# Kernel optimization log

Hardware: AMD Instinct MI355X
Metric: run time of the kernel (lower is better)

Reference implementation:

```python
import jax, jax.numpy as jnp
import numpy as np
from jax import lax

BN_EPS = 1e-5


def binary_activation(x):
    # STE: forward = sign(x), backward = piecewise polynomial approximation
    out_fwd = jnp.sign(x)
    m1 = (x < -1).astype(x.dtype)
    m2 = (x < 0).astype(x.dtype)
    m3 = (x < 1).astype(x.dtype)
    out1 = -1.0 * m1 + (x * x + 2 * x) * (1 - m1)
    out2 = out1 * m2 + (-x * x + 2 * x) * (1 - m2)
    out3 = out2 * m3 + 1.0 * (1 - m3)
    return lax.stop_gradient(out_fwd) - lax.stop_gradient(out3) + out3


def binarize_weight(w):
    # per-output-channel scale * sign(w), STE through clipped weights
    scale = lax.stop_gradient(jnp.mean(jnp.abs(w), axis=(1, 2, 3), keepdims=True))
    bw_ng = scale * jnp.sign(w)
    wc = jnp.clip(w, -1.0, 1.0)
    return lax.stop_gradient(bw_ng) - lax.stop_gradient(wc) + wc


def conv3x3(x, w):
    return lax.conv_general_dilated(
        x, w, window_strides=(1, 1), padding=((1, 1), (1, 1)),
        dimension_numbers=('NCHW', 'OIHW', 'NCHW'))


def shift4(x, amt):
    # chunk into 4 along channel; roll +-amt over H for first two, over W for last two
    x1, x2, x3, x4 = jnp.split(x, 4, axis=1)
    return jnp.concatenate([
        jnp.roll(x1, amt, axis=2),
        jnp.roll(x2, -amt, axis=2),
        jnp.roll(x3, amt, axis=3),
        jnp.roll(x4, -amt, axis=3),
    ], axis=1)


def setup_inputs() -> dict:
    key = jax.random.key(0)
    ks = jax.random.split(key, 8)
    B, C, H, W = 32, 256, 56, 56
    x = jax.random.normal(ks[0], (B, C, H, W), dtype=jnp.float32)
    w0 = jax.random.uniform(ks[1], (C, C, 3, 3), dtype=jnp.float32) * 0.001
    w1 = jax.random.uniform(ks[2], (C, C, 3, 3), dtype=jnp.float32) * 0.001
    w2 = jax.random.uniform(ks[3], (C, C, 3, 3), dtype=jnp.float32) * 0.001
    return {
        'x': x,
        'bias0': jnp.zeros((1, C, 1, 1), jnp.float32),
        'w0': w0, 'w1': w1, 'w2': w2,
        'gamma': jnp.ones((C,), jnp.float32),
        'beta': jnp.zeros((C,), jnp.float32),
        'rmean': jnp.zeros((C,), jnp.float32),
        'rvar': jnp.ones((C,), jnp.float32),
        'bias1': jnp.zeros((1, C, 1, 1), jnp.float32),
        'prelu_a': 0.25 * jnp.ones((C,), jnp.float32),
        'bias2': jnp.zeros((1, C, 1, 1), jnp.float32),
    }


def reference(x, bias0, w0, w1, w2, gamma, beta, rmean, rvar, bias1, prelu_a, bias2):
    residual = x
    out = binary_activation(x + bias0)
    out1 = conv3x3(out, binarize_weight(w0))
    out2 = conv3x3(shift4(out, 1), binarize_weight(w1))   # Shift: roll by 1
    out3 = conv3x3(shift4(out, 3), binarize_weight(w2))   # GlobalShift: roll by 3
    s = out1 + out2 + out3
    # BatchNorm2d (inference mode with running stats)
    c = (1, -1, 1, 1)
    bn = (s - rmean.reshape(c)) * (gamma.reshape(c) * lax.rsqrt(rvar.reshape(c) + BN_EPS)) + beta.reshape(c)
    out = bn + residual
    out = out + bias1
    a = prelu_a.reshape(c)
    out = jnp.where(out > 0, out, a * out)  # PReLU, per-channel slope
    out = out + bias2
    return out
```

## Files before the change

kernel.cpp:

```cpp
#include <hip/hip_runtime.h>
#include <stdint.h>

#define BB 32
#define CC 256
#define HH 56
#define WW 56
#define TAPS 9
#define NCONV 3
#define BN_EPS 1e-5f

typedef int   int4v __attribute__((ext_vector_type(4)));
typedef float f16v  __attribute__((ext_vector_type(16)));

#define MFMA_FP4(accv, av, bv) \
    asm("v_mfma_f32_32x32x64_f8f6f4 %0, %1, %2, %0 cbsz:4 blgp:4" \
        : "+v"(accv) : "v"(av), "v"(bv))

#define ACT4_BYTES ((size_t)BB * HH * WW * 128)
#define WPK4_BYTES ((size_t)NCONV * 8 * 4 * TAPS * 64 * 16)
#define OT4_STRIDE 36864

#define L_PX   32
#define L_ROW  (58 * L_PX)
#define L_G    (4 * L_ROW)
#define NST4   464
#define SWZ(c) ((((c) ^ ((c) >> 2)) & 3) << 4)

__global__ __launch_bounds__(256) void pack_act4_kernel(
    const float* __restrict__ x, const float* __restrict__ bias0,
    uint8_t* __restrict__ act4)
{
    __shared__ uint8_t nib[56 * 260];
    const int tid = threadIdx.x;
    const int h = blockIdx.x % HH, n = blockIdx.x / HH;
    const int w = tid & 63;
    const int cq = tid >> 6;
    if (w < WW) {
        #pragma unroll 4
        for (int cc = 0; cc < 64; ++cc) {
            const int c = cc * 4 + cq;
            const float v = x[((size_t)(n * CC + c) * HH + h) * WW + w] + bias0[c];
            nib[w * 260 + c] = (v > 0.f) ? 0x2 : ((v < 0.f) ? 0xA : 0x0);
        }
    }
    __syncthreads();
    uint32_t* o32 = (uint32_t*)(act4 + (size_t)(n * HH + h) * WW * 128);
    #pragma unroll
    for (int i = 0; i < 7; ++i) {
        const int flat = i * 1024 + tid * 4;
        const int ww = flat >> 7, b0 = flat & 127;
        uint32_t r = 0;
        #pragma unroll
        for (int k = 0; k < 4; ++k) {
            const int b = b0 + k;
            const uint32_t lo = nib[ww * 260 + 2 * b];
            const uint32_t hi = nib[ww * 260 + 2 * b + 1];
            r |= ((lo | (hi << 4)) & 0xFFu) << (8 * k);
        }
        o32[flat >> 2] = r;
    }
}

__global__ __launch_bounds__(64) void pack_scales_kernel(
    const float* __restrict__ w0, const float* __restrict__ w1,
    const float* __restrict__ w2, float* __restrict__ scales,
    const float* __restrict__ gamma, const float* __restrict__ beta,
    const float* __restrict__ rmean, const float* __restrict__ rvar,
    const float* __restrict__ bias1, const float* __restrict__ prelu_a,
    const float* __restrict__ bias2, float* __restrict__ epack)
{
    const int j = blockIdx.x >> 8;
    const int o = blockIdx.x & 255;
    const float* wp = (j == 0) ? w0 : ((j == 1) ? w1 : w2);
    const int lane = threadIdx.x;
    const float* wo = wp + (size_t)o * CC * TAPS;
    float s = 0.f;
    for (int k = lane; k < CC * TAPS; k += 64) s += fabsf(wo[k]);
    #pragma unroll
    for (int d = 32; d > 0; d >>= 1) s += __shfl_xor(s, d);
    if (lane == 0) scales[j * CC + o] = s * (1.0f / (float)(CC * TAPS));
    if (j == 0 && lane == 0) {
        const float A = gamma[o] * rsqrtf(rvar[o] + BN_EPS);
        epack[o * 4 + 0] = A;
        epack[o * 4 + 1] = beta[o] - rmean[o] * A + bias1[o];
        epack[o * 4 + 2] = prelu_a[o];
        epack[o * 4 + 3] = bias2[o];
    }
}

__global__ __launch_bounds__(256) void pack_wpk4_kernel(
    const float* __restrict__ w0, const float* __restrict__ w1,
    const float* __restrict__ w2, uint8_t* __restrict__ wpk)
{
    const int j  = blockIdx.x >> 3;
    const int ot = blockIdx.x & 7;
    const float* wp = (j == 0) ? w0 : ((j == 1) ? w1 : w2);
    #pragma unroll 1
    for (int it = 0; it < 9; ++it) {
        const int e = it * 256 + threadIdx.x;
        const int g = e / 576;
        const int rem = e % 576;
        const int t = rem >> 6;
        const int ln = rem & 63;
        const int o = ot * 32 + (ln & 31);
        const int chb = g * 64 + ((ln >> 5) & 1) * 32;
        uint8_t bytes[16];
        #pragma unroll
        for (int b = 0; b < 16; ++b) {
            const float vlo = wp[((size_t)o * CC + chb + 2 * b) * TAPS + t];
            const float vhi = wp[((size_t)o * CC + chb + 2 * b + 1) * TAPS + t];
            const uint8_t nlo = (vlo > 0.f) ? 0x2 : ((vlo < 0.f) ? 0xA : 0x0);
            const uint8_t nhi = (vhi > 0.f) ? 0x2 : ((vhi < 0.f) ? 0xA : 0x0);
            bytes[b] = (uint8_t)(nlo | (nhi << 4));
        }
        *(int4v*)(wpk + ((size_t)((j * 8 + ot) * 4 + g) * 9 + t) * 1024 + ln * 16)
            = *(const int4v*)bytes;
    }
}

__global__ __launch_bounds__(256) void conv_mfma4_kernel(
    const uint8_t* __restrict__ act4, const uint8_t* __restrict__ wpk,
    const float* __restrict__ scales, const float* __restrict__ epack,
    const float* __restrict__ x, float* __restrict__ out)
{
    __shared__ __align__(16) uint8_t lds[2][L_G];
    const int tid  = threadIdx.x;
    const int lane = tid & 63;
    const int wv   = __builtin_amdgcn_readfirstlane(tid >> 6);
    const int bid  = blockIdx.x;
    const int swz  = (bid & 7) * 196 + (bid >> 3);
    const int pxblk = swz % 49;
    const int n     = swz / 49;
    const int px0   = pxblk * 64;
    const int h_lo  = px0 / WW;

    int boff[2][3];
    #pragma unroll
    for (int pt = 0; pt < 2; ++pt) {
        const int p = px0 + pt * 32 + (lane & 31);
        const int hl = p / WW, wl = p % WW;
        #pragma unroll
        for (int tc = 0; tc < 3; ++tc) {
            const int col = wl + tc;
            const int a = (hl - h_lo) * L_ROW + col * L_PX + ((lane >> 5) & 1) * 16;
            boff[pt][tc] = a ^ SWZ(col);
        }
    }
    const size_t nbase = (size_t)n * HH;

    float fsum[2][2][16];
    #pragma unroll
    for (int q = 0; q < 2; ++q)
        #pragma unroll
        for (int pt = 0; pt < 2; ++pt)
            #pragma unroll
            for (int r = 0; r < 16; ++r) fsum[q][pt][r] = 0.f;

    f16v acc[2][2];
    int4v sreg[2];
    int4v Ar[3][2], Br[2][2];

    auto stage_load = [&](int jj, int gg) {
        const int amt = (jj == 0) ? 0 : ((jj == 1) ? 1 : 3);
        const int rH = (gg == 0) ? -amt : ((gg == 1) ? amt : 0);
        const int rW = (gg == 2) ? -amt : ((gg == 3) ? amt : 0);
        #pragma unroll
        for (int k = 0; k < 2; ++k) {
            const int u = tid + k * 256;
            int4v v = {0, 0, 0, 0};
            if (u < NST4) {
                const int r = u / 116;
                const int rem = u - r * 116;
                const int c = rem >> 1, q = rem & 1;
                const int hr = h_lo - 1 + r, wc = c - 1;
                if (hr >= 0 && hr < HH && wc >= 0 && wc < WW) {
                    int hs = hr + rH; if (hs < 0) hs += HH; else if (hs >= HH) hs -= HH;
                    int ws = wc + rW; if (ws < 0) ws += WW; else if (ws >= WW) ws -= WW;
                    v = *(const int4v*)(act4 +
                        (((nbase + hs) * WW + ws) << 7) + gg * 32 + q * 16);
                }
            }
            sreg[k] = v;
        }
    };
    auto stage_write = [&](uint8_t* Ln) {
        #pragma unroll
        for (int k = 0; k < 2; ++k) {
            const int u = tid + k * 256;
            if (u < NST4) {
                const int r = u / 116;
                const int rem = u - r * 116;
                const int c = rem >> 1, q = rem & 1;
                int a = r * L_ROW + c * L_PX + q * 16;
                a ^= SWZ(c);
                *(int4v*)(Ln + a) = sreg[k];
            }
        }
    };

#define LDA4(S, U) do { \
        Ar[S][0] = *(const int4v*)(wbase + (U) * 1024); \
        Ar[S][1] = *(const int4v*)(wbase + OT4_STRIDE + (U) * 1024); } while (0)
#define LDB4(S, U) do { \
        const int imm_ = ((U) / 3) * L_ROW; \
        const int tc_ = (U) % 3; \
        Br[S][0] = *(const int4v*)(L + boff[0][tc_] + imm_); \
        Br[S][1] = *(const int4v*)(L + boff[1][tc_] + imm_); } while (0)
#define MMX4(SA, SB) do { \
        MFMA_FP4(acc[0][0], Ar[SA][0], Br[SB][0]); \
        MFMA_FP4(acc[0][1], Ar[SA][0], Br[SB][1]); \
        MFMA_FP4(acc[1][0], Ar[SA][1], Br[SB][0]); \
        MFMA_FP4(acc[1][1], Ar[SA][1], Br[SB][1]); } while (0)

    stage_load(0, 0);
    stage_write(&lds[0][0]);
    {
        const uint8_t* wbase = wpk + ((size_t)((0 * 8 + wv * 2) * 4 + 0) * 9) * 1024
                             + lane * 16;
        LDA4(0, 0); LDA4(1, 1); LDA4(2, 2);
    }
    __syncthreads();

    #pragma unroll 1
    for (int ph = 0; ph < 12; ++ph) {
        const int j = ph >> 2, g = ph & 3;
        if ((ph & 3) == 0) {
            #pragma unroll
            for (int q = 0; q < 2; ++q)
                #pragma unroll
                for (int pt = 0; pt < 2; ++pt) acc[q][pt] = (f16v)0.f;
        }

        const uint8_t* L = &lds[ph & 1][0];
        const uint8_t* wbase = wpk
            + ((size_t)((j * 8 + wv * 2) * 4 + g) * 9) * 1024 + lane * 16;

        LDB4(0, 0); LDB4(1, 1);

        if (ph < 11) {
            const int ph2 = ph + 1;
            stage_load(ph2 >> 2, ph2 & 3);
        }

        __builtin_amdgcn_s_setprio(1);
        MMX4(0, 0); LDA4(0, 3); LDB4(0, 2);
        MMX4(1, 1); LDA4(1, 4); LDB4(1, 3);
        MMX4(2, 0); LDA4(2, 5); LDB4(0, 4);
        MMX4(0, 1); LDA4(0, 6); LDB4(1, 5);
        MMX4(1, 0); LDA4(1, 7); LDB4(0, 6);
        MMX4(2, 1); LDA4(2, 8); LDB4(1, 7);
        MMX4(0, 0);             LDB4(0, 8);
        MMX4(1, 1);
        MMX4(2, 0);
        __builtin_amdgcn_s_setprio(0);

        if (ph < 11) {
            const int ph2 = ph + 1;
            const int j2 = ph2 >> 2, g2 = ph2 & 3;
            const uint8_t* wbase = wpk
                + ((size_t)((j2 * 8 + wv * 2) * 4 + g2) * 9) * 1024 + lane * 16;
            LDA4(0, 0); LDA4(1, 1); LDA4(2, 2);
        }

        if (ph < 11) stage_write(&lds[(ph + 1) & 1][0]);

        if ((ph & 3) == 3) {
            const float* scj = scales + j * CC + wv * 64;
            #pragma unroll
            for (int q = 0; q < 2; ++q) {
                #pragma unroll
                for (int r = 0; r < 16; ++r) {
                    const int rb = q * 32 + (r & 3) + 8 * (r >> 2);
                    const float slo = scj[rb], shi = scj[rb + 4];
                    const float sc = (lane & 32) ? shi : slo;
                    fsum[q][0][r] += sc * acc[q][0][r];
                    fsum[q][1][r] += sc * acc[q][1][r];
                }
            }
        }
        __syncthreads();
    }
#undef LDA4
#undef LDB4
#undef MMX4

    const int voff = (lane & 31) + ((lane >> 5) & 1) * (4 * HH * WW);
    #pragma unroll
    for (int q = 0; q < 2; ++q) {
        #pragma unroll
        for (int r = 0; r < 16; ++r) {
            const int o_lo = wv * 64 + q * 32 + (r & 3) + 8 * (r >> 2);
            const float* elo = epack + o_lo * 4;
            const float* ehi = epack + (o_lo + 4) * 4;
            const bool hi = (lane & 32) != 0;
            const float e0 = hi ? ehi[0] : elo[0];
            const float e1 = hi ? ehi[1] : elo[1];
            const float e2 = hi ? ehi[2] : elo[2];
            const float e3 = hi ? ehi[3] : elo[3];
            const size_t base = ((size_t)n * CC + o_lo) * (HH * WW) + px0;
            #pragma unroll
            for (int pt = 0; pt < 2; ++pt) {
                const size_t off = base + pt * 32 + voff;
                float v = fsum[q][pt][r] * e0 + e1 + x[off];
                v = (v > 0.f) ? v : e2 * v;
                out[off] = v + e3;
            }
        }
    }
}

extern "C" void kernel_launch(void* const* d_in, const int* in_sizes, int n_in,
                              void* d_out, int out_size, void* d_ws, size_t ws_size,
                              hipStream_t stream) {
    const float* x       = (const float*)d_in[0];
    const float* bias0   = (const float*)d_in[1];
    const float* w0      = (const float*)d_in[2];
    const float* w1      = (const float*)d_in[3];
    const float* w2      = (const float*)d_in[4];
    const float* gamma   = (const float*)d_in[5];
    const float* beta    = (const float*)d_in[6];
    const float* rmean   = (const float*)d_in[7];
    const float* rvar    = (const float*)d_in[8];
    const float* bias1   = (const float*)d_in[9];
    const float* prelu_a = (const float*)d_in[10];
    const float* bias2   = (const float*)d_in[11];
    float* out = (float*)d_out;

    uint8_t* act4   = (uint8_t*)d_ws;
    uint8_t* wpk    = act4 + ACT4_BYTES;
    float*   scales = (float*)(wpk + WPK4_BYTES);
    float*   epack  = scales + NCONV * CC;

    pack_act4_kernel<<<dim3(BB * HH), dim3(256), 0, stream>>>(x, bias0, act4);
    pack_scales_kernel<<<dim3(NCONV * CC), dim3(64), 0, stream>>>(
        w0, w1, w2, scales, gamma, beta, rmean, rvar, bias1, prelu_a, bias2, epack);
    pack_wpk4_kernel<<<dim3(NCONV * 8), dim3(256), 0, stream>>>(w0, w1, w2, wpk);
    conv_mfma4_kernel<<<dim3(BB * 49), dim3(256), 0, stream>>>(
        act4, wpk, scales, epack, x, out);
}
```

Baseline: 203.5 us.

## Split conv block across 8 waves and stage two channel groups per phase

The conv kernel now launches 512 threads per block. Each wave handles one 32-pixel half of the tile for a 64-channel output slice instead of both halves, which halves the per-wave accumulators. Each pipeline phase stages two channel groups into LDS at once, cutting the phase count from 12 to 6 and the number of barriers accordingly. The cost is twice the LDS per block, which may reduce blocks per CU, and A-operand weight loads are now duplicated across the two pixel-half waves.

Measured after the change: 239.9 us. 17.9% more time.

```diff
diff --git a/kernel.cpp b/kernel.cpp
--- a/kernel.cpp
+++ b/kernel.cpp
@@ -23,7 +23,8 @@
 #define L_PX   32
 #define L_ROW  (58 * L_PX)
 #define L_G    (4 * L_ROW)
-#define NST4   464
+#define L_P2   (2 * L_G)
+#define NST2   928
 #define SWZ(c) ((((c) ^ ((c) >> 2)) & 3) << 4)
 
 __global__ __launch_bounds__(256) void pack_act4_kernel(
@@ -118,15 +119,17 @@
     }
 }
 
-__global__ __launch_bounds__(256) void conv_mfma4_kernel(
+__global__ __launch_bounds__(512) void conv_mfma4_kernel(
     const uint8_t* __restrict__ act4, const uint8_t* __restrict__ wpk,
     const float* __restrict__ scales, const float* __restrict__ epack,
     const float* __restrict__ x, float* __restrict__ out)
 {
-    __shared__ __align__(16) uint8_t lds[2][L_G];
+    __shared__ __align__(16) uint8_t lds[2][L_P2];
     const int tid  = threadIdx.x;
     const int lane = tid & 63;
     const int wv   = __builtin_amdgcn_readfirstlane(tid >> 6);
+    const int o2   = wv & 3;
+    const int pt   = wv >> 2;
     const int bid  = blockIdx.x;
     const int swz  = (bid & 7) * 196 + (bid >> 3);
     const int pxblk = swz % 49;
@@ -134,50 +137,50 @@
     const int px0   = pxblk * 64;
     const int h_lo  = px0 / WW;
 
-    int boff[2][3];
-    #pragma unroll
-    for (int pt = 0; pt < 2; ++pt) {
+    int boff[3];
+    {
         const int p = px0 + pt * 32 + (lane & 31);
         const int hl = p / WW, wl = p % WW;
         #pragma unroll
         for (int tc = 0; tc < 3; ++tc) {
             const int col = wl + tc;
             const int a = (hl - h_lo) * L_ROW + col * L_PX + ((lane >> 5) & 1) * 16;
-            boff[pt][tc] = a ^ SWZ(col);
+            boff[tc] = a ^ SWZ(col);
         }
     }
     const size_t nbase = (size_t)n * HH;
 
-    float fsum[2][2][16];
+    float fsum[2][16];
     #pragma unroll
     for (int q = 0; q < 2; ++q)
         #pragma unroll
-        for (int pt = 0; pt < 2; ++pt)
-            #pragma unroll
-            for (int r = 0; r < 16; ++r) fsum[q][pt][r] = 0.f;
-
-    f16v acc[2][2];
+        for (int r = 0; r < 16; ++r) fsum[q][r] = 0.f;
+
+    f16v acc[2];
     int4v sreg[2];
-    int4v Ar[3][2], Br[2][2];
-
-    auto stage_load = [&](int jj, int gg) {
+    int4v Ar[3][2], Br[3];
+
+    auto stage_load = [&](int jj, int gp) {
         const int amt = (jj == 0) ? 0 : ((jj == 1) ? 1 : 3);
-        const int rH = (gg == 0) ? -amt : ((gg == 1) ? amt : 0);
-        const int rW = (gg == 2) ? -amt : ((gg == 3) ? amt : 0);
         #pragma unroll
         for (int k = 0; k < 2; ++k) {
-            const int u = tid + k * 256;
+            const int u = tid + k * 512;
             int4v v = {0, 0, 0, 0};
-            if (u < NST4) {
-                const int r = u / 116;
-                const int rem = u - r * 116;
+            if (u < NST2) {
+                const int gl = u / 464;
+                const int vv = u - gl * 464;
+                const int r = vv / 116;
+                const int rem = vv - r * 116;
                 const int c = rem >> 1, q = rem & 1;
+                const int g = gp * 2 + gl;
+                const int rH = (g == 0) ? -amt : ((g == 1) ? amt : 0);
+                const int rW = (g == 2) ? -amt : ((g == 3) ? amt : 0);
                 const int hr = h_lo - 1 + r, wc = c - 1;
                 if (hr >= 0 && hr < HH && wc >= 0 && wc < WW) {
                     int hs = hr + rH; if (hs < 0) hs += HH; else if (hs >= HH) hs -= HH;
                     int ws = wc + rW; if (ws < 0) ws += WW; else if (ws >= WW) ws -= WW;
                     v = *(const int4v*)(act4 +
-                        (((nbase + hs) * WW + ws) << 7) + gg * 32 + q * 16);
+                        (((nbase + hs) * WW + ws) << 7) + g * 32 + q * 16);
                 }
             }
             sreg[k] = v;
@@ -186,12 +189,14 @@
     auto stage_write = [&](uint8_t* Ln) {
         #pragma unroll
         for (int k = 0; k < 2; ++k) {
-            const int u = tid + k * 256;
-            if (u < NST4) {
-                const int r = u / 116;
-                const int rem = u - r * 116;
+            const int u = tid + k * 512;
+            if (u < NST2) {
+                const int gl = u / 464;
+                const int vv = u - gl * 464;
+                const int r = vv / 116;
+                const int rem = vv - r * 116;
                 const int c = rem >> 1, q = rem & 1;
-                int a = r * L_ROW + c * L_PX + q * 16;
+                int a = gl * L_G + r * L_ROW + c * L_PX + q * 16;
                 a ^= SWZ(c);
                 *(int4v*)(Ln + a) = sreg[k];
             }
@@ -202,79 +207,78 @@
         Ar[S][0] = *(const int4v*)(wbase + (U) * 1024); \
         Ar[S][1] = *(const int4v*)(wbase + OT4_STRIDE + (U) * 1024); } while (0)
 #define LDB4(S, U) do { \
-        const int imm_ = ((U) / 3) * L_ROW; \
-        const int tc_ = (U) % 3; \
-        Br[S][0] = *(const int4v*)(L + boff[0][tc_] + imm_); \
-        Br[S][1] = *(const int4v*)(L + boff[1][tc_] + imm_); } while (0)
-#define MMX4(SA, SB) do { \
-        MFMA_FP4(acc[0][0], Ar[SA][0], Br[SB][0]); \
-        MFMA_FP4(acc[0][1], Ar[SA][0], Br[SB][1]); \
-        MFMA_FP4(acc[1][0], Ar[SA][1], Br[SB][0]); \
-        MFMA_FP4(acc[1][1], Ar[SA][1], Br[SB][1]); } while (0)
+        const int gl_ = (U) / 9, t_ = (U) % 9; \
+        const int imm_ = gl_ * L_G + (t_ / 3) * L_ROW; \
+        Br[S] = *(const int4v*)(L + boff[t_ % 3] + imm_); } while (0)
+#define MMX4(S) do { \
+        MFMA_FP4(acc[0], Ar[S][0], Br[S]); \
+        MFMA_FP4(acc[1], Ar[S][1], Br[S]); } while (0)
 
     stage_load(0, 0);
     stage_write(&lds[0][0]);
     {
-        const uint8_t* wbase = wpk + ((size_t)((0 * 8 + wv * 2) * 4 + 0) * 9) * 1024
-                             + lane * 16;
+        const uint8_t* wbase = wpk
+            + ((size_t)((0 * 8 + o2 * 2) * 4 + 0) * 9) * 1024 + lane * 16;
         LDA4(0, 0); LDA4(1, 1); LDA4(2, 2);
     }
     __syncthreads();
 
     #pragma unroll 1
-    for (int ph = 0; ph < 12; ++ph) {
-        const int j = ph >> 2, g = ph & 3;
-        if ((ph & 3) == 0) {
-            #pragma unroll
-            for (int q = 0; q < 2; ++q)
-                #pragma unroll
-                for (int pt = 0; pt < 2; ++pt) acc[q][pt] = (f16v)0.f;
-        }
+    for (int ph = 0; ph < 6; ++ph) {
+        const int j = ph >> 1, gp = ph & 1;
+        if (gp == 0) { acc[0] = (f16v)0.f; acc[1] = (f16v)0.f; }
 
         const uint8_t* L = &lds[ph & 1][0];
         const uint8_t* wbase = wpk
-            + ((size_t)((j * 8 + wv * 2) * 4 + g) * 9) * 1024 + lane * 16;
-
-        LDB4(0, 0); LDB4(1, 1);
-
-        if (ph < 11) {
+            + ((size_t)((j * 8 + o2 * 2) * 4 + gp * 2) * 9) * 1024 + lane * 16;
+
+        LDB4(0, 0); LDB4(1, 1); LDB4(2, 2);
+
+        if (ph < 5) {
             const int ph2 = ph + 1;
-            stage_load(ph2 >> 2, ph2 & 3);
+            stage_load(ph2 >> 1, ph2 & 1);
         }
 
         __builtin_amdgcn_s_setprio(1);
-        MMX4(0, 0); LDA4(0, 3); LDB4(0, 2);
-        MMX4(1, 1); LDA4(1, 4); LDB4(1, 3);
-        MMX4(2, 0); LDA4(2, 5); LDB4(0, 4);
-        MMX4(0, 1); LDA4(0, 6); LDB4(1, 5);
-        MMX4(1, 0); LDA4(1, 7); LDB4(0, 6);
-        MMX4(2, 1); LDA4(2, 8); LDB4(1, 7);
-        MMX4(0, 0);             LDB4(0, 8);
-        MMX4(1, 1);
-        MMX4(2, 0);
+        MMX4(0); LDA4(0, 3);  LDB4(0, 3);
+        MMX4(1); LDA4(1, 4);  LDB4(1, 4);
+        MMX4(2); LDA4(2, 5);  LDB4(2, 5);
+        MMX4(0); LDA4(0, 6);  LDB4(0, 6);
+        MMX4(1); LDA4(1, 7);  LDB4(1, 7);
+        MMX4(2); LDA4(2, 8);  LDB4(2, 8);
+        MMX4(0); LDA4(0, 9);  LDB4(0, 9);
+        MMX4(1); LDA4(1, 10); LDB4(1, 10);
+        MMX4(2); LDA4(2, 11); LDB4(2, 11);
+        MMX4(0); LDA4(0, 12); LDB4(0, 12);
+        MMX4(1); LDA4(1, 13); LDB4(1, 13);
+        MMX4(2); LDA4(2, 14); LDB4(2, 14);
+        MMX4(0); LDA4(0, 15); LDB4(0, 15);
+        MMX4(1); LDA4(1, 16); LDB4(1, 16);
+        MMX4(2); LDA4(2, 17); LDB4(2, 17);
+        MMX4(0);
+        MMX4(1);
+        MMX4(2);
         __builtin_amdgcn_s_setprio(0);
 
-        if (ph < 11) {
+        if (ph < 5) {
             const int ph2 = ph + 1;
-            const int j2 = ph2 >> 2, g2 = ph2 & 3;
+            const int j2 = ph2 >> 1, gp2 = ph2 & 1;
             const uint8_t* wbase = wpk
-                + ((size_t)((j2 * 8 + wv * 2) * 4 + g2) * 9) * 1024 + lane * 16;
+                + ((size_t)((j2 * 8 + o2 * 2) * 4 + gp2 * 2) * 9) * 1024 + lane * 16;
             LDA4(0, 0); LDA4(1, 1); LDA4(2, 2);
         }
 
-        if (ph < 11) stage_write(&lds[(ph + 1) & 1][0]);
-
-        if ((ph & 3) == 3) {
-            const float* scj = scales + j * CC + wv * 64;
+        if (ph < 5) stage_write(&lds[(ph + 1) & 1][0]);
+
+        if (gp == 1) {
+            const float* scj = scales + j * CC + o2 * 64;
             #pragma unroll
             for (int q = 0; q < 2; ++q) {
                 #pragma unroll
                 for (int r = 0; r < 16; ++r) {
                     const int rb = q * 32 + (r & 3) + 8 * (r >> 2);
-                    const float slo = scj[rb], shi = scj[rb + 4];
-                    const float sc = (lane & 32) ? shi : slo;
-                    fsum[q][0][r] += sc * acc[q][0][r];
-                    fsum[q][1][r] += sc * acc[q][1][r];
+                    const float sc = (lane & 32) ? scj[rb + 4] : scj[rb];
+                    fsum[q][r] += sc * acc[q][r];
                 }
             }
         }
@@ -289,7 +293,7 @@
     for (int q = 0; q < 2; ++q) {
         #pragma unroll
         for (int r = 0; r < 16; ++r) {
-            const int o_lo = wv * 64 + q * 32 + (r & 3) + 8 * (r >> 2);
+            const int o_lo = o2 * 64 + q * 32 + (r & 3) + 8 * (r >> 2);
             const float* elo = epack + o_lo * 4;
             const float* ehi = epack + (o_lo + 4) * 4;
             const bool hi = (lane & 32) != 0;
@@ -297,14 +301,11 @@
             const float e1 = hi ? ehi[1] : elo[1];
             const float e2 = hi ? ehi[2] : elo[2];
             const float e3 = hi ? ehi[3] : elo[3];
-            const size_t base = ((size_t)n * CC + o_lo) * (HH * WW) + px0;
-            #pragma unroll
-            for (int pt = 0; pt < 2; ++pt) {
-                const size_t off = base + pt * 32 + voff;
-                float v = fsum[q][pt][r] * e0 + e1 + x[off];
-                v = (v > 0.f) ? v : e2 * v;
-                out[off] = v + e3;
-            }
+            const size_t off = ((size_t)n * CC + o_lo) * (HH * WW)
+                             + px0 + pt * 32 + voff;
+            float v = fsum[q][r] * e0 + e1 + x[off];
+            v = (v > 0.f) ? v : e2 * v;
+            out[off] = v + e3;
         }
     }
 }
@@ -335,6 +336,6 @@
     pack_scales_kernel<<<dim3(NCONV * CC), dim3(64), 0, stream>>>(
         w0, w1, w2, scales, gamma, beta, rmean, rvar, bias1, prelu_a, bias2, epack);
     pack_wpk4_kernel<<<dim3(NCONV * 8), dim3(256), 0, stream>>>(w0, w1, w2, wpk);
-    conv_mfma4_kernel<<<dim3(BB * 49), dim3(256), 0, stream>>>(
+    conv_mfma4_kernel<<<dim3(BB * 49), dim3(512), 0, stream>>>(
         act4, wpk, scales, epack, x, out);
 }
```
